# Kernel tuning notes

Measured on AMD Instinct MI355X. Metric: run time of the kernel, lower is better.

## Reference

```python
import jax, jax.numpy as jnp
import numpy as np

B, E, WIN, DX, DZ, RAW = 2048, 32, 10, 14, 14, 22

def _leaky(x):
    return jnp.where(x >= 0, x, 0.01 * x)

def setup_inputs():
    key = jax.random.key(0)
    ks = jax.random.split(key, 20)
    def w(k, i, o):
        return jax.random.normal(k, (i, o), dtype=jnp.float32) / np.float32(np.sqrt(i))
    def b(k, o):
        return jax.random.normal(k, (o,), dtype=jnp.float32) * 0.01
    return {
        "raw_obs": jax.random.normal(ks[0], (B, WIN, 1, RAW), dtype=jnp.float32),
        "state_prev": jax.random.normal(ks[1], (B, E, WIN, DX), dtype=jnp.float32),
        "pm_w1": w(ks[2], WIN * DX, 256), "pm_b1": b(ks[3], 256),
        "pm_w3": w(ks[4], 256, 512), "pm_b3": b(ks[5], 512),
        "pm_wm2": w(ks[6], 512, DX), "pm_bm2": b(ks[7], DX),
        "sm_w2": w(ks[8], WIN * RAW, 256), "sm_b2": b(ks[9], 256),
        "sm_w3": w(ks[10], 256, 256), "sm_b3": b(ks[11], 256),
        "sm_w5": w(ks[12], 256, 64), "sm_b5": b(ks[13], 64),
        "sm_w6": w(ks[14], 64, DZ), "sm_b6": b(ks[15], DZ),
        "on_w1": w(ks[16], DZ, 32), "on_b1": b(ks[17], 32),
        "on_w2": w(ks[18], 32, DZ), "on_b2": b(ks[19], DZ),
    }

def reference(raw_obs, state_prev, pm_w1, pm_b1, pm_w3, pm_b3, pm_wm2, pm_bm2,
              sm_w2, sm_b2, sm_w3, sm_b3, sm_w5, sm_b5, sm_w6, sm_b6,
              on_w1, on_b1, on_w2, on_b2):
    bs, ens, win, dx = state_prev.shape
    dz = sm_w6.shape[1]
    # --- process model (LinearFlipout evaluated at mean weights) ---
    x = state_prev.reshape(bs * ens, win * dx)
    x = _leaky(x @ pm_w1 + pm_b1)
    x = _leaky(x @ pm_w3 + pm_b3)
    state_pred = (x @ pm_wm2 + pm_bm2).reshape(bs, ens, dx)   # [B,E,dx]
    state_m = state_pred.mean(axis=1)                          # [B,dx]
    A = state_pred - state_m[:, None, :]                       # [B,E,dx]
    # --- sensor model: torch repeat(E,1,1,1) tiles ensemble-major, the final
    # reshape reinterprets as batch-major; replicate that layout faithfully ---
    s = jnp.tile(raw_obs, (ens, 1, 1, 1)).reshape(bs * ens, win * raw_obs.shape[-1])
    s = _leaky(s @ sm_w2 + sm_b2)
    s = _leaky(s @ sm_w3 + sm_b3)
    s = _leaky(s @ sm_w5 + sm_b5)
    s = s @ sm_w6 + sm_b6
    ensemble_z = s.reshape(bs, ens, dz)                        # [B,E,dz]
    z = ensemble_z.mean(axis=1, keepdims=True)                 # [B,1,dz]
    # --- observation noise R = diag_embed(square(mlp(z)+c) + init) ---
    r = jax.nn.relu(z @ on_w1 + on_b1) @ on_w2 + on_b2
    r = jnp.square(r + 0.001) + 0.038729833
    R = r.reshape(bs, dz)[:, :, None] * jnp.eye(dz, dtype=r.dtype)  # [B,dz,dz]
    # --- EnKF correction ---
    S = jnp.einsum('bei,bej->bij', A, A)                       # AT @ A, [B,dx,dx]
    innovation = S / (ens - 1) + R
    K = (S / (ens - 1)) @ jnp.linalg.inv(innovation)           # [B,dx,dz]
    diff = ensemble_z - state_pred                             # (y - H_XT)^T, [B,E,dz]
    gain = jnp.einsum('bij,bej->bei', K, diff)                 # [B,E,dx]
    state_corrected = state_pred + gain
    return (state_corrected,
            state_corrected.mean(axis=1, keepdims=True),
            state_m[:, None, :],
            z,
            ensemble_z)
```

## Files before the change

kernel.cpp:

```cpp
#include <hip/hip_runtime.h>

typedef unsigned short u16;
typedef __attribute__((ext_vector_type(8))) short short8;
typedef __attribute__((ext_vector_type(4))) float floatx4;

#define MFMA_BF16 __builtin_amdgcn_mfma_f32_16x16x32_bf16

__device__ __forceinline__ u16 f2bf(float f) {
    union { float f; unsigned int i; } v; v.f = f;
    unsigned int u = v.i;
    u += 0x7fffu + ((u >> 16) & 1u);
    return (u16)(u >> 16);
}
__device__ __forceinline__ float leaky(float x) { return x >= 0.f ? x : 0.01f * x; }

#define H1S 264
#define RS 232
#define XS 168
#define H3S 72

#define O1 917504
#define O2 946176
#define O3 974848
#define O4 1003520

#define PW1   0
#define PW3   40960
#define PWM2  172032
#define PSW2  180224
#define PSW3  237568
#define PSW5  303104
#define PSW6  319488
#define PTOTAL 320512
#define WS_NEEDED 641024
#define WS_BIG (641024 + 3670016)

struct PackSeg { const float* W; int K, N, S, base, count; };
struct PackArgs { PackSeg seg[7]; };

__global__ __launch_bounds__(256) void pack_all(PackArgs pa, u16* __restrict__ P) {
    int u = blockIdx.x * 256 + threadIdx.x;
    if (u >= PTOTAL) return;
#pragma unroll
    for (int i = 0; i < 7; i++) {
        if (u >= pa.seg[i].base && u < pa.seg[i].base + pa.seg[i].count) {
            int v = u - pa.seg[i].base;
            int j = v & 7;
            int l = (v >> 3) & 63;
            int ts = v >> 9;
            int s = ts % pa.seg[i].S;
            int t = ts / pa.seg[i].S;
            int k = s * 32 + (l >> 4) * 8 + j;
            int n = t * 16 + (l & 15);
            P[u] = (k < pa.seg[i].K && n < pa.seg[i].N)
                       ? f2bf(pa.seg[i].W[k * pa.seg[i].N + n]) : (u16)0;
            return;
        }
    }
}

__global__ __launch_bounds__(512, 2) void merged_mlp(
    const float* __restrict__ Rg, const float* __restrict__ Xg,
    const u16* __restrict__ Pk,
    const float* __restrict__ b1, const float* __restrict__ b3,
    const float* __restrict__ bm2,
    const float* __restrict__ b2, const float* __restrict__ sb3,
    const float* __restrict__ b5, const float* __restrict__ b6,
    float* __restrict__ ez_out,
    float* __restrict__ sp_ws)
{
    __shared__ __align__(16) u16 ldsH[128 * H1S];
    __shared__ __align__(16) u16 ldsC[128 * H1S];

    const int tid  = threadIdx.x;
    const int lane = tid & 63;
    const int wave = tid >> 6;
    const int q    = lane >> 4;
    const int n16  = lane & 15;
    const int rh   = wave >> 2;
    const int cg   = wave & 3;

    if (blockIdx.x < 32) {
        const u16* w2p = Pk + PSW2;
        const u16* w3p = Pk + PSW3;
        const u16* w5p = Pk + PSW5;
        const u16* w6p = Pk + PSW6;
        const int row0 = blockIdx.x * 64;

        for (int idx = tid; idx < 64 * 56; idx += 512) {
            int r = idx / 56, c4 = idx - r * 56;
            float4 v = {0.f, 0.f, 0.f, 0.f};
            if (c4 < 55) v = *(const float4*)&Rg[(row0 + r) * 220 + c4 * 4];
            u16* dst = &ldsH[r * RS + c4 * 4];
            dst[0] = f2bf(v.x); dst[1] = f2bf(v.y); dst[2] = f2bf(v.z); dst[3] = f2bf(v.w);
        }
        __syncthreads();

        floatx4 acc1[4][2];
        {
            floatx4 zero = {0.f, 0.f, 0.f, 0.f};
#pragma unroll
            for (int rt = 0; rt < 4; rt++)
#pragma unroll
                for (int ct = 0; ct < 2; ct++) acc1[rt][ct] = zero;
#pragma unroll
            for (int s = 0; s < 7; s++) {
                short8 a[4];
#pragma unroll
                for (int rt = 0; rt < 4; rt++)
                    a[rt] = *(const short8*)&ldsH[(rt * 16 + n16) * RS + s * 32 + q * 8];
#pragma unroll
                for (int ct = 0; ct < 2; ct++) {
                    int t = wave * 2 + ct;
                    short8 bf = *(const short8*)&w2p[((t * 7 + s) * 64 + lane) * 8];
#pragma unroll
                    for (int rt = 0; rt < 4; rt++)
                        acc1[rt][ct] = MFMA_BF16(a[rt], bf, acc1[rt][ct], 0, 0, 0);
                }
            }
        }
        __syncthreads();
#pragma unroll
        for (int ct = 0; ct < 2; ct++) {
            int col = (wave * 2 + ct) * 16 + n16;
            float bias = b2[col];
#pragma unroll
            for (int rt = 0; rt < 4; rt++)
#pragma unroll
                for (int r = 0; r < 4; r++)
                    ldsH[(rt * 16 + q * 4 + r) * H1S + col] = f2bf(leaky(acc1[rt][ct][r] + bias));
        }
        __syncthreads();

        {
            floatx4 zero = {0.f, 0.f, 0.f, 0.f};
            floatx4 acc[4][2];
#pragma unroll
            for (int rt = 0; rt < 4; rt++)
#pragma unroll
                for (int ct = 0; ct < 2; ct++) acc[rt][ct] = zero;
#pragma unroll
            for (int s = 0; s < 8; s++) {
                short8 a[4];
#pragma unroll
                for (int rt = 0; rt < 4; rt++)
                    a[rt] = *(const short8*)&ldsH[(rt * 16 + n16) * H1S + s * 32 + q * 8];
#pragma unroll
                for (int ct = 0; ct < 2; ct++) {
                    int t = wave * 2 + ct;
                    short8 bf = *(const short8*)&w3p[((t * 8 + s) * 64 + lane) * 8];
#pragma unroll
                    for (int rt = 0; rt < 4; rt++)
                        acc[rt][ct] = MFMA_BF16(a[rt], bf, acc[rt][ct], 0, 0, 0);
                }
            }
#pragma unroll
            for (int ct = 0; ct < 2; ct++) {
                int cl = (wave * 2 + ct) * 16 + n16;
                float bias = sb3[cl];
#pragma unroll
                for (int rt = 0; rt < 4; rt++)
#pragma unroll
                    for (int r = 0; r < 4; r++)
                        ldsC[(rt * 16 + q * 4 + r) * H1S + cl] = f2bf(leaky(acc[rt][ct][r] + bias));
            }
        }
        __syncthreads();

        floatx4 acc5[4];
        {
            floatx4 zero = {0.f, 0.f, 0.f, 0.f};
#pragma unroll
            for (int rt = 0; rt < 4; rt++) acc5[rt] = zero;
            int t5 = wave >> 1, sh = wave & 1;
#pragma unroll
            for (int u = 0; u < 4; u++) {
                int s = sh * 4 + u;
                short8 bf = *(const short8*)&w5p[((t5 * 8 + s) * 64 + lane) * 8];
#pragma unroll
                for (int rt = 0; rt < 4; rt++) {
                    short8 a = *(const short8*)&ldsC[(rt * 16 + n16) * H1S + s * 32 + q * 8];
                    acc5[rt] = MFMA_BF16(a, bf, acc5[rt], 0, 0, 0);
                }
            }
        }
        {
            float* pacc = (float*)ldsH;
            int p = wave & 1, t5 = wave >> 1;
#pragma unroll
            for (int rt = 0; rt < 4; rt++)
#pragma unroll
                for (int r = 0; r < 4; r++)
                    pacc[(p * 64 + rt * 16 + q * 4 + r) * 64 + t5 * 16 + n16] = acc5[rt][r];
        }
        __syncthreads();

        {
            const float* pacc = (const float*)ldsH;
            for (int idx = tid; idx < 4096; idx += 512) {
                int row = idx >> 6, col = idx & 63;
                float v = pacc[row * 64 + col] + pacc[(64 + row) * 64 + col];
                ldsC[row * H3S + col] = f2bf(leaky(v + b5[col]));
            }
        }
        __syncthreads();

        {
            floatx4 zero = {0.f, 0.f, 0.f, 0.f};
            floatx4 acc = zero;
            int s = wave & 1, rq = wave >> 1;
            short8 bf = *(const short8*)&w6p[(s * 64 + lane) * 8];
            short8 a = *(const short8*)&ldsC[(rq * 16 + n16) * H3S + s * 32 + q * 8];
            acc = MFMA_BF16(a, bf, acc, 0, 0, 0);
            float* pacc2 = (float*)ldsH;
#pragma unroll
            for (int r = 0; r < 4; r++)
                pacc2[(s * 64 + rq * 16 + q * 4 + r) * 16 + n16] = acc[r];
        }
        __syncthreads();
        {
            const float* pacc2 = (const float*)ldsH;
            for (int idx = tid; idx < 1024; idx += 512) {
                int r = idx >> 4, c = idx & 15;
                float v = pacc2[idx] + pacc2[1024 + idx];
                if (c < 14) ez_out[(row0 + r) * 14 + c] = v + b6[c];
            }
        }
    } else {
        const u16* w1p  = Pk + PW1;
        const u16* w3p  = Pk + PW3;
        const u16* wm2p = Pk + PWM2;
        const int bb   = blockIdx.x - 32;
        const int row0 = bb * 128;

        for (int idx = tid; idx < 128 * 42; idx += 512) {
            int r = idx / 42, c4 = idx - r * 42;
            float4 v = {0.f, 0.f, 0.f, 0.f};
            if (c4 < 35) v = *(const float4*)&Xg[(row0 + r) * 140 + c4 * 4];
            u16* dst = &ldsH[r * XS + c4 * 4];
            dst[0] = f2bf(v.x); dst[1] = f2bf(v.y); dst[2] = f2bf(v.z); dst[3] = f2bf(v.w);
        }
        __syncthreads();

        floatx4 acc1[4][4];
        {
            floatx4 zero = {0.f, 0.f, 0.f, 0.f};
#pragma unroll
            for (int rt = 0; rt < 4; rt++)
#pragma unroll
                for (int ct = 0; ct < 4; ct++) acc1[rt][ct] = zero;
#pragma unroll
            for (int s = 0; s < 5; s++) {
                short8 a[4];
#pragma unroll
                for (int rt = 0; rt < 4; rt++)
                    a[rt] = *(const short8*)&ldsH[(rh * 64 + rt * 16 + n16) * XS + s * 32 + q * 8];
#pragma unroll
                for (int ct = 0; ct < 4; ct++) {
                    int t = cg * 4 + ct;
                    short8 bf = *(const short8*)&w1p[((t * 5 + s) * 64 + lane) * 8];
#pragma unroll
                    for (int rt = 0; rt < 4; rt++)
                        acc1[rt][ct] = MFMA_BF16(a[rt], bf, acc1[rt][ct], 0, 0, 0);
                }
            }
        }
        __syncthreads();
#pragma unroll
        for (int ct = 0; ct < 4; ct++) {
            int col = (cg * 4 + ct) * 16 + n16;
            float bias = b1[col];
#pragma unroll
            for (int rt = 0; rt < 4; rt++)
#pragma unroll
                for (int r = 0; r < 4; r++)
                    ldsH[(rh * 64 + rt * 16 + q * 4 + r) * H1S + col] = f2bf(leaky(acc1[rt][ct][r] + bias));
        }
        __syncthreads();

        floatx4 acc3[4];
        {
            floatx4 zero = {0.f, 0.f, 0.f, 0.f};
#pragma unroll
            for (int rt = 0; rt < 4; rt++) acc3[rt] = zero;
        }
#pragma unroll
        for (int c = 0; c < 2; c++) {
            floatx4 zero = {0.f, 0.f, 0.f, 0.f};
            floatx4 acc[4][4];
#pragma unroll
            for (int rt = 0; rt < 4; rt++)
#pragma unroll
                for (int ct = 0; ct < 4; ct++) acc[rt][ct] = zero;
#pragma unroll
            for (int s = 0; s < 8; s++) {
                short8 a[4];
#pragma unroll
                for (int rt = 0; rt < 4; rt++)
                    a[rt] = *(const short8*)&ldsH[(rh * 64 + rt * 16 + n16) * H1S + s * 32 + q * 8];
#pragma unroll
                for (int ct = 0; ct < 4; ct++) {
                    int tg = c * 16 + cg * 4 + ct;
                    short8 bf = *(const short8*)&w3p[((tg * 8 + s) * 64 + lane) * 8];
#pragma unroll
                    for (int rt = 0; rt < 4; rt++)
                        acc[rt][ct] = MFMA_BF16(a[rt], bf, acc[rt][ct], 0, 0, 0);
                }
            }
#pragma unroll
            for (int ct = 0; ct < 4; ct++) {
                int cl = (cg * 4 + ct) * 16 + n16;
                float bias = b3[c * 256 + cl];
#pragma unroll
                for (int rt = 0; rt < 4; rt++)
#pragma unroll
                    for (int r = 0; r < 4; r++)
                        ldsC[(rh * 64 + rt * 16 + q * 4 + r) * H1S + cl] = f2bf(leaky(acc[rt][ct][r] + bias));
            }
            __syncthreads();
#pragma unroll
            for (int uu = 0; uu < 2; uu++) {
                int u = cg * 2 + uu;
                short8 bf = *(const short8*)&wm2p[((c * 8 + u) * 64 + lane) * 8];
#pragma unroll
                for (int rt = 0; rt < 4; rt++) {
                    short8 a = *(const short8*)&ldsC[(rh * 64 + rt * 16 + n16) * H1S + u * 32 + q * 8];
                    acc3[rt] = MFMA_BF16(a, bf, acc3[rt], 0, 0, 0);
                }
            }
            __syncthreads();
        }

        {
            float* pacc = (float*)ldsH;
#pragma unroll
            for (int rt = 0; rt < 4; rt++)
#pragma unroll
                for (int r = 0; r < 4; r++)
                    pacc[(cg * 128 + rh * 64 + rt * 16 + q * 4 + r) * 16 + n16] = acc3[rt][r];
        }
        __syncthreads();
        {
            const float* pacc = (const float*)ldsH;
            for (int idx = tid; idx < 2048; idx += 512) {
                int r = idx >> 4, c = idx & 15;
                float v = pacc[idx] + pacc[2048 + idx] + pacc[4096 + idx] + pacc[6144 + idx];
                if (c < 14) sp_ws[(row0 + r) * 14 + c] = v + bm2[c];
            }
        }
    }
}

__global__ __launch_bounds__(256) void enkf_tail(
    const float* __restrict__ sp_all,
    const float* __restrict__ on_w1, const float* __restrict__ on_b1,
    const float* __restrict__ on_w2, const float* __restrict__ on_b2,
    float* out)
{
    __shared__ float spv[32][14];
    __shared__ float ezv[32][14];
    __shared__ float smv[14], zzv[14], rrv[14];
    __shared__ float M[14][14];
    __shared__ float G[14][28];
    __shared__ float Kmat[14][14];
    __shared__ float fac[14];
    __shared__ float hbuf[32];

    const int tid = threadIdx.x;
    const int b = blockIdx.x;

    for (int idx = tid; idx < 448; idx += 256) ((float*)spv)[idx] = sp_all[b * 448 + idx];
    {
        const float* ezsrc = out + O4 + (b & 63) * 448;
        for (int idx = tid; idx < 448; idx += 256) ((float*)ezv)[idx] = ezsrc[idx];
    }
    __syncthreads();

    if (tid < 14) {
        float s = 0.f;
        for (int e = 0; e < 32; e++) s += spv[e][tid];
        smv[tid] = s * (1.f / 32.f);
    } else if (tid >= 32 && tid < 46) {
        int c = tid - 32;
        float s = 0.f;
        for (int e = 0; e < 32; e++) s += ezv[e][c];
        zzv[c] = s * (1.f / 32.f);
    }
    __syncthreads();

    if (tid < 196) {
        int i = tid / 14, j = tid - i * 14;
        float mi = smv[i], mj = smv[j];
        float s = 0.f;
        for (int e = 0; e < 32; e++) s += (spv[e][i] - mi) * (spv[e][j] - mj);
        M[i][j] = s * (1.f / 31.f);
    } else if (tid >= 224) {
        int l = tid - 224;
        float t = on_b1[l];
        for (int k = 0; k < 14; k++) t += zzv[k] * on_w1[k * 32 + l];
        hbuf[l] = t > 0.f ? t : 0.f;
    }
    __syncthreads();

    if (tid < 14) {
        float t = on_b2[tid];
        for (int k = 0; k < 32; k++) t += hbuf[k] * on_w2[k * 14 + tid];
        t += 0.001f;
        rrv[tid] = t * t + 0.038729833f;
    }
    __syncthreads();

    for (int idx = tid; idx < 392; idx += 256) {
        int i = idx / 28, j = idx - i * 28;
        G[i][j] = (j < 14) ? (M[i][j] + (i == j ? rrv[i] : 0.f))
                           : ((j - 14 == i) ? 1.f : 0.f);
    }
    __syncthreads();

    for (int c = 0; c < 14; c++) {
        if (tid < 64) {
            float pinv = 1.f / G[c][c];
            if (tid < 28) G[c][tid] *= pinv;
            if (tid < 14 && tid != c) fac[tid] = G[tid][c];
        }
        __syncthreads();
        for (int idx = tid; idx < 392; idx += 256) {
            int i = idx / 28, j = idx - i * 28;
            if (i != c) G[i][j] -= fac[i] * G[c][j];
        }
        __syncthreads();
    }

    if (tid < 196) {
        int i = tid / 14, j = tid - i * 14;
        float s = 0.f;
        for (int k = 0; k < 14; k++) s += M[i][k] * G[k][14 + j];
        Kmat[i][j] = s;
    }
    __syncthreads();

    for (int idx = tid; idx < 448; idx += 256) {
        int e = idx / 14, i = idx - e * 14;
        float g = 0.f;
        for (int j = 0; j < 14; j++) g += Kmat[i][j] * (ezv[e][j] - spv[e][j]);
        out[b * 448 + idx] = spv[e][i] + g;
        out[O4 + b * 448 + idx] = ezv[e][i];
    }
    if (tid < 14) {
        float g = 0.f;
        for (int j = 0; j < 14; j++) g += Kmat[tid][j] * (zzv[j] - smv[j]);
        out[O1 + b * 14 + tid] = smv[tid] + g;
        out[O2 + b * 14 + tid] = smv[tid];
        out[O3 + b * 14 + tid] = zzv[tid];
    }
}

extern "C" void kernel_launch(void* const* d_in, const int* in_sizes, int n_in,
                              void* d_out, int out_size, void* d_ws, size_t ws_size,
                              hipStream_t stream) {
    (void)in_sizes; (void)n_in; (void)out_size; (void)ws_size;

    const float* raw_obs    = (const float*)d_in[0];
    const float* state_prev = (const float*)d_in[1];
    const float* pm_w1  = (const float*)d_in[2];
    const float* pm_b1  = (const float*)d_in[3];
    const float* pm_w3  = (const float*)d_in[4];
    const float* pm_b3  = (const float*)d_in[5];
    const float* pm_wm2 = (const float*)d_in[6];
    const float* pm_bm2 = (const float*)d_in[7];
    const float* sm_w2  = (const float*)d_in[8];
    const float* sm_b2  = (const float*)d_in[9];
    const float* sm_w3  = (const float*)d_in[10];
    const float* sm_b3  = (const float*)d_in[11];
    const float* sm_w5  = (const float*)d_in[12];
    const float* sm_b5  = (const float*)d_in[13];
    const float* sm_w6  = (const float*)d_in[14];
    const float* sm_b6  = (const float*)d_in[15];
    const float* on_w1  = (const float*)d_in[16];
    const float* on_b1  = (const float*)d_in[17];
    const float* on_w2  = (const float*)d_in[18];
    const float* on_b2  = (const float*)d_in[19];

    float* out = (float*)d_out;
    u16* P = (u16*)d_ws;
    float* sp_ws = (float*)((char*)d_ws + WS_NEEDED);

    PackArgs pa;
    pa.seg[0] = { pm_w1,  140, 256, 5,  PW1,  40960  };
    pa.seg[1] = { pm_w3,  256, 512, 8,  PW3,  131072 };
    pa.seg[2] = { pm_wm2, 512, 14,  16, PWM2, 8192   };
    pa.seg[3] = { sm_w2,  220, 256, 7,  PSW2, 57344  };
    pa.seg[4] = { sm_w3,  256, 256, 8,  PSW3, 65536  };
    pa.seg[5] = { sm_w5,  256, 64,  8,  PSW5, 16384  };
    pa.seg[6] = { sm_w6,  64,  14,  2,  PSW6, 1024   };
    pack_all<<<(PTOTAL + 255) / 256, 256, 0, stream>>>(pa, P);

    merged_mlp<<<544, 512, 0, stream>>>(raw_obs, state_prev, P,
                                        pm_b1, pm_b3, pm_bm2,
                                        sm_b2, sm_b3, sm_b5, sm_b6,
                                        out + O4, sp_ws);
    enkf_tail<<<2048, 256, 0, stream>>>(sp_ws, on_w1, on_b1, on_w2, on_b2, out);
}
```

Baseline: 179.0 us.

## Shrink merged MLP blocks to 256 threads and 64 rows, doubling grid

The merged MLP kernel now runs 256-thread blocks that each handle 64 rows instead of 512-thread blocks handling 128 rows. The process-model branch goes from 512 to 1024 blocks, and the whole grid from 544 to 1056. Each wave now covers more output columns: four tiles in the sensor layers, and a full K loop for layer 5, which drops one partial-sum reduction pass and a barrier. LDS per block halves, which allows more resident blocks and better load balance across CUs. The cost is more accumulator registers per wave and weight fragments re-read by twice as many blocks.

```diff
diff --git a/kernel.cpp b/kernel.cpp
--- a/kernel.cpp
+++ b/kernel.cpp
@@ -59,7 +59,7 @@
     }
 }
 
-__global__ __launch_bounds__(512, 2) void merged_mlp(
+__global__ __launch_bounds__(256, 2) void merged_mlp(
     const float* __restrict__ Rg, const float* __restrict__ Xg,
     const u16* __restrict__ Pk,
     const float* __restrict__ b1, const float* __restrict__ b3,
@@ -69,16 +69,14 @@
     float* __restrict__ ez_out,
     float* __restrict__ sp_ws)
 {
-    __shared__ __align__(16) u16 ldsH[128 * H1S];
-    __shared__ __align__(16) u16 ldsC[128 * H1S];
+    __shared__ __align__(16) u16 ldsH[64 * H1S];
+    __shared__ __align__(16) u16 ldsC[64 * H1S];
 
     const int tid  = threadIdx.x;
     const int lane = tid & 63;
     const int wave = tid >> 6;
     const int q    = lane >> 4;
     const int n16  = lane & 15;
-    const int rh   = wave >> 2;
-    const int cg   = wave & 3;
 
     if (blockIdx.x < 32) {
         const u16* w2p = Pk + PSW2;
@@ -87,7 +85,7 @@
         const u16* w6p = Pk + PSW6;
         const int row0 = blockIdx.x * 64;
 
-        for (int idx = tid; idx < 64 * 56; idx += 512) {
+        for (int idx = tid; idx < 64 * 56; idx += 256) {
             int r = idx / 56, c4 = idx - r * 56;
             float4 v = {0.f, 0.f, 0.f, 0.f};
             if (c4 < 55) v = *(const float4*)&Rg[(row0 + r) * 220 + c4 * 4];
@@ -96,13 +94,13 @@
         }
         __syncthreads();
 
-        floatx4 acc1[4][2];
-        {
-            floatx4 zero = {0.f, 0.f, 0.f, 0.f};
-#pragma unroll
-            for (int rt = 0; rt < 4; rt++)
-#pragma unroll
-                for (int ct = 0; ct < 2; ct++) acc1[rt][ct] = zero;
+        floatx4 acc1[4][4];
+        {
+            floatx4 zero = {0.f, 0.f, 0.f, 0.f};
+#pragma unroll
+            for (int rt = 0; rt < 4; rt++)
+#pragma unroll
+                for (int ct = 0; ct < 4; ct++) acc1[rt][ct] = zero;
 #pragma unroll
             for (int s = 0; s < 7; s++) {
                 short8 a[4];
@@ -110,8 +108,8 @@
                 for (int rt = 0; rt < 4; rt++)
                     a[rt] = *(const short8*)&ldsH[(rt * 16 + n16) * RS + s * 32 + q * 8];
 #pragma unroll
-                for (int ct = 0; ct < 2; ct++) {
-                    int t = wave * 2 + ct;
+                for (int ct = 0; ct < 4; ct++) {
+                    int t = wave * 4 + ct;
                     short8 bf = *(const short8*)&w2p[((t * 7 + s) * 64 + lane) * 8];
 #pragma unroll
                     for (int rt = 0; rt < 4; rt++)
@@ -121,8 +119,8 @@
         }
         __syncthreads();
 #pragma unroll
-        for (int ct = 0; ct < 2; ct++) {
-            int col = (wave * 2 + ct) * 16 + n16;
+        for (int ct = 0; ct < 4; ct++) {
+            int col = (wave * 4 + ct) * 16 + n16;
             float bias = b2[col];
 #pragma unroll
             for (int rt = 0; rt < 4; rt++)
@@ -134,11 +132,11 @@
 
         {
             floatx4 zero = {0.f, 0.f, 0.f, 0.f};
-            floatx4 acc[4][2];
-#pragma unroll
-            for (int rt = 0; rt < 4; rt++)
-#pragma unroll
-                for (int ct = 0; ct < 2; ct++) acc[rt][ct] = zero;
+            floatx4 acc[4][4];
+#pragma unroll
+            for (int rt = 0; rt < 4; rt++)
+#pragma unroll
+                for (int ct = 0; ct < 4; ct++) acc[rt][ct] = zero;
 #pragma unroll
             for (int s = 0; s < 8; s++) {
                 short8 a[4];
@@ -146,8 +144,8 @@
                 for (int rt = 0; rt < 4; rt++)
                     a[rt] = *(const short8*)&ldsH[(rt * 16 + n16) * H1S + s * 32 + q * 8];
 #pragma unroll
-                for (int ct = 0; ct < 2; ct++) {
-                    int t = wave * 2 + ct;
+                for (int ct = 0; ct < 4; ct++) {
+                    int t = wave * 4 + ct;
                     short8 bf = *(const short8*)&w3p[((t * 8 + s) * 64 + lane) * 8];
 #pragma unroll
                     for (int rt = 0; rt < 4; rt++)
@@ -155,8 +153,8 @@
                 }
             }
 #pragma unroll
-            for (int ct = 0; ct < 2; ct++) {
-                int cl = (wave * 2 + ct) * 16 + n16;
+            for (int ct = 0; ct < 4; ct++) {
+                int cl = (wave * 4 + ct) * 16 + n16;
                 float bias = sb3[cl];
 #pragma unroll
                 for (int rt = 0; rt < 4; rt++)
@@ -172,11 +170,9 @@
             floatx4 zero = {0.f, 0.f, 0.f, 0.f};
 #pragma unroll
             for (int rt = 0; rt < 4; rt++) acc5[rt] = zero;
-            int t5 = wave >> 1, sh = wave & 1;
-#pragma unroll
-            for (int u = 0; u < 4; u++) {
-                int s = sh * 4 + u;
-                short8 bf = *(const short8*)&w5p[((t5 * 8 + s) * 64 + lane) * 8];
+#pragma unroll
+            for (int s = 0; s < 8; s++) {
+                short8 bf = *(const short8*)&w5p[((wave * 8 + s) * 64 + lane) * 8];
 #pragma unroll
                 for (int rt = 0; rt < 4; rt++) {
                     short8 a = *(const short8*)&ldsC[(rt * 16 + n16) * H1S + s * 32 + q * 8];
@@ -185,42 +181,37 @@
             }
         }
         {
-            float* pacc = (float*)ldsH;
-            int p = wave & 1, t5 = wave >> 1;
+            int col = wave * 16 + n16;
+            float bias = b5[col];
 #pragma unroll
             for (int rt = 0; rt < 4; rt++)
 #pragma unroll
                 for (int r = 0; r < 4; r++)
-                    pacc[(p * 64 + rt * 16 + q * 4 + r) * 64 + t5 * 16 + n16] = acc5[rt][r];
-        }
-        __syncthreads();
-
-        {
-            const float* pacc = (const float*)ldsH;
-            for (int idx = tid; idx < 4096; idx += 512) {
-                int row = idx >> 6, col = idx & 63;
-                float v = pacc[row * 64 + col] + pacc[(64 + row) * 64 + col];
-                ldsC[row * H3S + col] = f2bf(leaky(v + b5[col]));
-            }
-        }
-        __syncthreads();
-
-        {
-            floatx4 zero = {0.f, 0.f, 0.f, 0.f};
-            floatx4 acc = zero;
-            int s = wave & 1, rq = wave >> 1;
+                    ldsH[(rt * 16 + q * 4 + r) * H3S + col] = f2bf(leaky(acc5[rt][r] + bias));
+        }
+        __syncthreads();
+
+        {
+            floatx4 zero = {0.f, 0.f, 0.f, 0.f};
+            floatx4 acc6[2] = {zero, zero};
+            int s = wave & 1, rh2 = wave >> 1;
             short8 bf = *(const short8*)&w6p[(s * 64 + lane) * 8];
-            short8 a = *(const short8*)&ldsC[(rq * 16 + n16) * H3S + s * 32 + q * 8];
-            acc = MFMA_BF16(a, bf, acc, 0, 0, 0);
-            float* pacc2 = (float*)ldsH;
-#pragma unroll
-            for (int r = 0; r < 4; r++)
-                pacc2[(s * 64 + rq * 16 + q * 4 + r) * 16 + n16] = acc[r];
-        }
-        __syncthreads();
-        {
-            const float* pacc2 = (const float*)ldsH;
-            for (int idx = tid; idx < 1024; idx += 512) {
+#pragma unroll
+            for (int rt = 0; rt < 2; rt++) {
+                short8 a = *(const short8*)&ldsH[(rh2 * 32 + rt * 16 + n16) * H3S + s * 32 + q * 8];
+                acc6[rt] = MFMA_BF16(a, bf, acc6[rt], 0, 0, 0);
+            }
+            float* pacc2 = (float*)ldsC;
+#pragma unroll
+            for (int rt = 0; rt < 2; rt++)
+#pragma unroll
+                for (int r = 0; r < 4; r++)
+                    pacc2[(s * 64 + rh2 * 32 + rt * 16 + q * 4 + r) * 16 + n16] = acc6[rt][r];
+        }
+        __syncthreads();
+        {
+            const float* pacc2 = (const float*)ldsC;
+            for (int idx = tid; idx < 1024; idx += 256) {
                 int r = idx >> 4, c = idx & 15;
                 float v = pacc2[idx] + pacc2[1024 + idx];
                 if (c < 14) ez_out[(row0 + r) * 14 + c] = v + b6[c];
@@ -231,9 +222,9 @@
         const u16* w3p  = Pk + PW3;
         const u16* wm2p = Pk + PWM2;
         const int bb   = blockIdx.x - 32;
-        const int row0 = bb * 128;
-
-        for (int idx = tid; idx < 128 * 42; idx += 512) {
+        const int row0 = bb * 64;
+
+        for (int idx = tid; idx < 64 * 42; idx += 256) {
             int r = idx / 42, c4 = idx - r * 42;
             float4 v = {0.f, 0.f, 0.f, 0.f};
             if (c4 < 35) v = *(const float4*)&Xg[(row0 + r) * 140 + c4 * 4];
@@ -254,10 +245,10 @@
                 short8 a[4];
 #pragma unroll
                 for (int rt = 0; rt < 4; rt++)
-                    a[rt] = *(const short8*)&ldsH[(rh * 64 + rt * 16 + n16) * XS + s * 32 + q * 8];
+                    a[rt] = *(const short8*)&ldsH[(rt * 16 + n16) * XS + s * 32 + q * 8];
 #pragma unroll
                 for (int ct = 0; ct < 4; ct++) {
-                    int t = cg * 4 + ct;
+                    int t = wave * 4 + ct;
                     short8 bf = *(const short8*)&w1p[((t * 5 + s) * 64 + lane) * 8];
 #pragma unroll
                     for (int rt = 0; rt < 4; rt++)
@@ -268,13 +259,13 @@
         __syncthreads();
 #pragma unroll
         for (int ct = 0; ct < 4; ct++) {
-            int col = (cg * 4 + ct) * 16 + n16;
+            int col = (wave * 4 + ct) * 16 + n16;
             float bias = b1[col];
 #pragma unroll
             for (int rt = 0; rt < 4; rt++)
 #pragma unroll
                 for (int r = 0; r < 4; r++)
-                    ldsH[(rh * 64 + rt * 16 + q * 4 + r) * H1S + col] = f2bf(leaky(acc1[rt][ct][r] + bias));
+                    ldsH[(rt * 16 + q * 4 + r) * H1S + col] = f2bf(leaky(acc1[rt][ct][r] + bias));
         }
         __syncthreads();
 
@@ -297,10 +288,10 @@
                 short8 a[4];
 #pragma unroll
                 for (int rt = 0; rt < 4; rt++)
-                    a[rt] = *(const short8*)&ldsH[(rh * 64 + rt * 16 + n16) * H1S + s * 32 + q * 8];
+                    a[rt] = *(const short8*)&ldsH[(rt * 16 + n16) * H1S + s * 32 + q * 8];
 #pragma unroll
                 for (int ct = 0; ct < 4; ct++) {
-                    int tg = c * 16 + cg * 4 + ct;
+                    int tg = c * 16 + wave * 4 + ct;
                     short8 bf = *(const short8*)&w3p[((tg * 8 + s) * 64 + lane) * 8];
 #pragma unroll
                     for (int rt = 0; rt < 4; rt++)
@@ -309,22 +300,22 @@
             }
 #pragma unroll
             for (int ct = 0; ct < 4; ct++) {
-                int cl = (cg * 4 + ct) * 16 + n16;
+                int cl = (wave * 4 + ct) * 16 + n16;
                 float bias = b3[c * 256 + cl];
 #pragma unroll
                 for (int rt = 0; rt < 4; rt++)
 #pragma unroll
                     for (int r = 0; r < 4; r++)
-                        ldsC[(rh * 64 + rt * 16 + q * 4 + r) * H1S + cl] = f2bf(leaky(acc[rt][ct][r] + bias));
+                        ldsC[(rt * 16 + q * 4 + r) * H1S + cl] = f2bf(leaky(acc[rt][ct][r] + bias));
             }
             __syncthreads();
 #pragma unroll
             for (int uu = 0; uu < 2; uu++) {
-                int u = cg * 2 + uu;
-                short8 bf = *(const short8*)&wm2p[((c * 8 + u) * 64 + lane) * 8];
+                int sgl = wave * 2 + uu;
+                short8 bf = *(const short8*)&wm2p[((c * 8 + sgl) * 64 + lane) * 8];
 #pragma unroll
                 for (int rt = 0; rt < 4; rt++) {
-                    short8 a = *(const short8*)&ldsC[(rh * 64 + rt * 16 + n16) * H1S + u * 32 + q * 8];
+                    short8 a = *(const short8*)&ldsC[(rt * 16 + n16) * H1S + sgl * 32 + q * 8];
                     acc3[rt] = MFMA_BF16(a, bf, acc3[rt], 0, 0, 0);
                 }
             }
@@ -337,14 +328,14 @@
             for (int rt = 0; rt < 4; rt++)
 #pragma unroll
                 for (int r = 0; r < 4; r++)
-                    pacc[(cg * 128 + rh * 64 + rt * 16 + q * 4 + r) * 16 + n16] = acc3[rt][r];
+                    pacc[(wave * 64 + rt * 16 + q * 4 + r) * 16 + n16] = acc3[rt][r];
         }
         __syncthreads();
         {
             const float* pacc = (const float*)ldsH;
-            for (int idx = tid; idx < 2048; idx += 512) {
+            for (int idx = tid; idx < 1024; idx += 256) {
                 int r = idx >> 4, c = idx & 15;
-                float v = pacc[idx] + pacc[2048 + idx] + pacc[4096 + idx] + pacc[6144 + idx];
+                float v = pacc[idx] + pacc[1024 + idx] + pacc[2048 + idx] + pacc[3072 + idx];
                 if (c < 14) sp_ws[(row0 + r) * 14 + c] = v + bm2[c];
             }
         }
@@ -495,9 +486,9 @@
     pa.seg[6] = { sm_w6,  64,  14,  2,  PSW6, 1024   };
     pack_all<<<(PTOTAL + 255) / 256, 256, 0, stream>>>(pa, P);
 
-    merged_mlp<<<544, 512, 0, stream>>>(raw_obs, state_prev, P,
-                                        pm_b1, pm_b3, pm_bm2,
-                                        sm_b2, sm_b3, sm_b5, sm_b6,
-                                        out + O4, sp_ws);
+    merged_mlp<<<1056, 256, 0, stream>>>(raw_obs, state_prev, P,
+                                         pm_b1, pm_b3, pm_bm2,
+                                         sm_b2, sm_b3, sm_b5, sm_b6,
+                                         out + O4, sp_ws);
     enkf_tail<<<2048, 256, 0, stream>>>(sp_ws, on_w1, on_b1, on_w2, on_b2, out);
 }
```

After: 186.0 us. 1.04x slower.
